# Kernel tuning notes

Hardware: AMD Instinct MI355X
Metric: run time of the kernel (lower is better)

Reference implementation:

```python
import jax, jax.numpy as jnp
import numpy as np

C_S, C_P, FEAT_DIM, NUM_BINS = 256, 128, 64, 22
TOTAL_EDGE_FEATS = FEAT_DIM * 2 + NUM_BINS * 2 + 2  # embed_diffuse_mask=True
LN_EPS = 1e-5


def calc_distogram(pos, min_bin, max_bin, num_bins):
    # pos: [B, N, 3] -> one-hot distance bins [B, N, N, num_bins]
    d = jnp.linalg.norm(pos[:, :, None, :] - pos[:, None, :, :], axis=-1)[..., None]
    lower = jnp.linspace(min_bin, max_bin, num_bins, dtype=pos.dtype)
    upper = jnp.concatenate([lower[1:], jnp.array([1e8], dtype=pos.dtype)])
    return ((d > lower) & (d < upper)).astype(pos.dtype)


def cross_concat(f):
    # f: [B, N, D] -> [B, N, N, 2D]: row-broadcast feats then col-broadcast feats
    B, N, D = f.shape
    fi = jnp.broadcast_to(f[:, :, None, :], (B, N, N, D))
    fj = jnp.broadcast_to(f[:, None, :, :], (B, N, N, D))
    return jnp.concatenate([fi, fj], axis=-1)


def setup_inputs() -> dict:
    key = jax.random.key(0)
    ks = jax.random.split(key, 12)
    B, N = 2, 512
    inp = {
        'init_node_embed': jax.random.normal(ks[0], (B, N, C_S), jnp.float32),
        'trans_t': jax.random.normal(ks[1], (B, N, 3), jnp.float32),
        'trans_sc': jax.random.normal(ks[2], (B, N, 3), jnp.float32),
        'edge_mask': jnp.ones((B, N, N), jnp.float32),
        'diffuse_mask': jnp.ones((B, N), jnp.float32),
        # params (fan-in scaled)
        'Wsp': jax.random.normal(ks[3], (C_S, FEAT_DIM), jnp.float32) / np.sqrt(C_S),
        'bsp': jnp.zeros((FEAT_DIM,), jnp.float32),
        'W1': jax.random.normal(ks[4], (TOTAL_EDGE_FEATS, C_P), jnp.float32) / np.sqrt(TOTAL_EDGE_FEATS),
        'b1': jnp.zeros((C_P,), jnp.float32),
        'W2': jax.random.normal(ks[5], (C_P, C_P), jnp.float32) / np.sqrt(C_P),
        'b2': jnp.zeros((C_P,), jnp.float32),
        'W3': jax.random.normal(ks[6], (C_P, C_P), jnp.float32) / np.sqrt(C_P),
        'b3': jnp.zeros((C_P,), jnp.float32),
        'ln_g': jnp.ones((C_P,), jnp.float32),
        'ln_b': jnp.zeros((C_P,), jnp.float32),
    }
    return inp


def reference(init_node_embed, trans_t, trans_sc, edge_mask, diffuse_mask,
              Wsp, bsp, W1, b1, W2, b2, W3, b3, ln_g, ln_b):
    p_i = init_node_embed @ Wsp + bsp                      # [B,N,feat_dim]
    cross_node = cross_concat(p_i)                          # [B,N,N,2*feat_dim]
    dist_feats = calc_distogram(trans_t, 1e-3, 20.0, NUM_BINS)
    sc_feats = calc_distogram(trans_sc, 1e-3, 20.0, NUM_BINS)
    diff_feat = cross_concat(diffuse_mask[..., None])       # [B,N,N,2]
    feats = jnp.concatenate([cross_node, dist_feats, sc_feats, diff_feat], axis=-1)
    h = jax.nn.relu(feats @ W1 + b1)
    h = jax.nn.relu(h @ W2 + b2)
    h = h @ W3 + b3
    mu = jnp.mean(h, axis=-1, keepdims=True)
    var = jnp.mean(jnp.square(h - mu), axis=-1, keepdims=True)
    h = (h - mu) * jax.lax.rsqrt(var + LN_EPS) * ln_g + ln_b
    return h * edge_mask[..., None]
```

## Files before the change

### kernel.cpp

```cpp
#include <hip/hip_runtime.h>
#include <hip/hip_bf16.h>
#include <math.h>

#define NB 2
#define NN 512
#define CS 256
#define CP 128
#define FD 64
#define NBINS 22
#define EPB 64

typedef __attribute__((ext_vector_type(8))) short bf16x8;
typedef __attribute__((ext_vector_type(4))) short bf16x4;
typedef __attribute__((ext_vector_type(4))) float f32x4;

__device__ __forceinline__ unsigned short f2bf_rne(float x) {
    unsigned int u = __float_as_uint(x);
    unsigned int r = (u + 0x7fffu + ((u >> 16) & 1u)) >> 16;
    return (unsigned short)r;
}
__device__ __forceinline__ float bf2f(unsigned short b) {
    return __uint_as_float(((unsigned int)b) << 16);
}
__device__ __forceinline__ unsigned short f2bf(float x) {
    __hip_bfloat16 h = __float2bfloat16(x);
    unsigned short u;
    __builtin_memcpy(&u, &h, 2);
    return u;
}

__device__ __forceinline__ int bin_of(float d, float step) {
    const float fk = __fdiv_rn(__fsub_rn(d, 0.001f), step);
    int k0 = (int)fk;
    k0 = k0 < 1 ? 1 : (k0 > 20 ? 20 : k0);
    int row = -1;
    #pragma unroll
    for (int dk = -1; dk <= 1; ++dk) {
        const int k = k0 + dk;
        const float lo = __fadd_rn(0.001f, __fmul_rn((float)k, step));
        const float hi = (k == NBINS - 1)
                       ? 1e8f
                       : __fadd_rn(0.001f, __fmul_rn((float)(k + 1), step));
        row = (d > lo && d < hi) ? k : row;
    }
    return row;
}

__global__ __launch_bounds__(256) void ef_prep_kernel(
    const float* __restrict__ x,
    const float* __restrict__ diffuse,
    const float* __restrict__ Wsp,
    const float* __restrict__ bsp,
    const float* __restrict__ W1,
    const float* __restrict__ b1,
    const float* __restrict__ W2,
    const float* __restrict__ W3,
    float* __restrict__ qr,
    unsigned short* __restrict__ Wp)
{
    __shared__ float xs[CS];
    __shared__ float ps[FD];
    const int t = threadIdx.x;
    if (blockIdx.x < 1024) {
        const int n = blockIdx.x;
        xs[t] = x[(size_t)n * CS + t];
        __syncthreads();
        if (t < FD) {
            float acc = bsp[t];
            #pragma unroll 8
            for (int k = 0; k < CS; ++k)
                acc = fmaf(xs[k], Wsp[k * FD + t], acc);
            ps[t] = acc;
        }
        __syncthreads();
        const float dm = diffuse[n];
        const int c = t & (CP - 1);
        if (t < CP) {
            float acc = b1[c] + dm * W1[172 * CP + c];
            #pragma unroll 8
            for (int k = 0; k < FD; ++k)
                acc = fmaf(ps[k], W1[k * CP + c], acc);
            qr[(size_t)n * CP + c] = acc;
        } else {
            float acc = dm * W1[173 * CP + c];
            #pragma unroll 8
            for (int k = 0; k < FD; ++k)
                acc = fmaf(ps[k], W1[(FD + k) * CP + c], acc);
            qr[(size_t)(1024 + n) * CP + c] = acc;
        }
    } else {
        const int s = (blockIdx.x - 1024) * 256 + t;
        const int j    = s & 7;
        const int lane = (s >> 3) & 63;
        const int mt   = (s >> 9) & 7;
        const int ki   = s >> 12;
        const int k = 32 * ki + 8 * (lane >> 4) + j;
        const int n = 16 * mt + (lane & 15);
        const float w2 = W2[k * CP + n];
        const float w3 = W3[k * CP + n];
        const unsigned short h2 = f2bf_rne(w2);
        const unsigned short l2 = f2bf_rne(w2 - bf2f(h2));
        const unsigned short h3 = f2bf_rne(w3);
        const unsigned short l3 = f2bf_rne(w3 - bf2f(h3));
        Wp[s]         = h2;
        Wp[16384 + s] = l2;
        Wp[32768 + s] = h3;
        Wp[49152 + s] = l3;
    }
}

__global__ __launch_bounds__(256, 4) void ef_edge_kernel(
    const float* __restrict__ trans_t,
    const float* __restrict__ trans_sc,
    const float* __restrict__ edge_mask,
    const float* __restrict__ W1,
    const float* __restrict__ b2,
    const float* __restrict__ b3,
    const float* __restrict__ ln_g,
    const float* __restrict__ ln_b,
    const float* __restrict__ qr,
    const unsigned short* __restrict__ Wp,
    float* __restrict__ out)
{
    __shared__ char hb8[32768];
    char* h1buf = hb8;
    char* h2buf = hb8 + 16384;
    float* psum_s  = (float*)hb8;
    float* pqsum_s = (float*)(hb8 + 4352);
    float* mus     = (float*)(hb8 + 8704);
    float* invs    = (float*)(hb8 + 8960);

    const int t   = threadIdx.x;
    const int blk = blockIdx.x;
    const int jt  = blk & 7;
    const int i   = (blk >> 3) & (NN - 1);
    const int b   = blk >> 12;
    const int j0  = jt * EPB;
    const int nodeI  = b * NN + i;
    const int nodeJ0 = b * NN + j0;

    const int w  = t >> 6;
    const int l  = t & 63;
    const int lr = l & 15;
    const int lg = l >> 4;
    const int e1 = t >> 2;
    const int c0 = (t & 3) * 32;
    const int nj = nodeJ0 + e1;

    const float step = __fdiv_rn(__fsub_rn(20.0f, 0.001f), 21.0f);
    float dx = __fsub_rn(trans_t[nodeI * 3 + 0], trans_t[nj * 3 + 0]);
    float dy = __fsub_rn(trans_t[nodeI * 3 + 1], trans_t[nj * 3 + 1]);
    float dz = __fsub_rn(trans_t[nodeI * 3 + 2], trans_t[nj * 3 + 2]);
    const float dT = sqrtf(__fadd_rn(__fadd_rn(__fmul_rn(dx, dx), __fmul_rn(dy, dy)), __fmul_rn(dz, dz)));
    dx = __fsub_rn(trans_sc[nodeI * 3 + 0], trans_sc[nj * 3 + 0]);
    dy = __fsub_rn(trans_sc[nodeI * 3 + 1], trans_sc[nj * 3 + 1]);
    dz = __fsub_rn(trans_sc[nodeI * 3 + 2], trans_sc[nj * 3 + 2]);
    const float dS = sqrtf(__fadd_rn(__fadd_rn(__fmul_rn(dx, dx), __fmul_rn(dy, dy)), __fmul_rn(dz, dz)));
    const int kT = bin_of(dT, step);
    const int kS = bin_of(dS, step);

    {
        const float fT = (kT < 0) ? 0.0f : 1.0f;
        const float fS = (kS < 0) ? 0.0f : 1.0f;
        const float* qrow = qr + (size_t)nodeI * CP + c0;
        const float* rrow = qr + (size_t)(1024 + nj) * CP + c0;
        const float* wTr  = W1 + (size_t)(kT < 0 ? 0 : 128 + kT) * CP + c0;
        const float* wSr  = W1 + (size_t)(kS < 0 ? 0 : 150 + kS) * CP + c0;
        #pragma unroll
        for (int ch = 0; ch < 4; ++ch) {
            const int cc = ch * 8;
            const float4 qa = *(const float4*)(qrow + cc);
            const float4 qb = *(const float4*)(qrow + cc + 4);
            const float4 ra = *(const float4*)(rrow + cc);
            const float4 rb = *(const float4*)(rrow + cc + 4);
            const float4 ta = *(const float4*)(wTr + cc);
            const float4 tb = *(const float4*)(wTr + cc + 4);
            const float4 sa = *(const float4*)(wSr + cc);
            const float4 sb = *(const float4*)(wSr + cc + 4);
            float h[8];
            h[0] = fmaxf(qa.x + ra.x + fT * ta.x + fS * sa.x, 0.0f);
            h[1] = fmaxf(qa.y + ra.y + fT * ta.y + fS * sa.y, 0.0f);
            h[2] = fmaxf(qa.z + ra.z + fT * ta.z + fS * sa.z, 0.0f);
            h[3] = fmaxf(qa.w + ra.w + fT * ta.w + fS * sa.w, 0.0f);
            h[4] = fmaxf(qb.x + rb.x + fT * tb.x + fS * sb.x, 0.0f);
            h[5] = fmaxf(qb.y + rb.y + fT * tb.y + fS * sb.y, 0.0f);
            h[6] = fmaxf(qb.z + rb.z + fT * tb.z + fS * sb.z, 0.0f);
            h[7] = fmaxf(qb.w + rb.w + fT * tb.w + fS * sb.w, 0.0f);
            bf16x8 H;
            #pragma unroll
            for (int u = 0; u < 8; ++u)
                H[u] = (short)f2bf(h[u]);
            const unsigned int ad = (unsigned int)e1 * 256 +
                (((unsigned int)(2 * (c0 + cc))) ^ (((unsigned int)e1 & 7) << 4));
            *(bf16x8*)(h1buf + ad) = H;
        }
    }
    __syncthreads();

    f32x4 acc[2][4];
    #pragma unroll
    for (int mt = 0; mt < 2; ++mt) {
        const float4 bv = *(const float4*)&b2[16 * (2 * w + mt) + 4 * lg];
        #pragma unroll
        for (int nt = 0; nt < 4; ++nt) {
            acc[mt][nt][0] = bv.x; acc[mt][nt][1] = bv.y;
            acc[mt][nt][2] = bv.z; acc[mt][nt][3] = bv.w;
        }
    }
    #pragma unroll
    for (int ki = 0; ki < 4; ++ki) {
        bf16x8 ah[2], al[2];
        #pragma unroll
        for (int mt = 0; mt < 2; ++mt) {
            const size_t off = (((size_t)ki * 8 + (2 * w + mt)) * 64 + l) * 8;
            ah[mt] = *(const bf16x8*)(Wp + off);
            al[mt] = *(const bf16x8*)(Wp + 16384 + off);
        }
        bf16x8 bh[4];
        #pragma unroll
        for (int nt = 0; nt < 4; ++nt) {
            const int e = 16 * nt + lr;
            const unsigned int ad = (unsigned int)e * 256 +
                (((unsigned int)(64 * ki + 16 * lg)) ^ (((unsigned int)e & 7) << 4));
            bh[nt] = *(const bf16x8*)(h1buf + ad);
        }
        __builtin_amdgcn_s_setprio(1);
        #pragma unroll
        for (int mt = 0; mt < 2; ++mt)
            #pragma unroll
            for (int nt = 0; nt < 4; ++nt) {
                acc[mt][nt] = __builtin_amdgcn_mfma_f32_16x16x32_bf16(ah[mt], bh[nt], acc[mt][nt], 0, 0, 0);
                acc[mt][nt] = __builtin_amdgcn_mfma_f32_16x16x32_bf16(al[mt], bh[nt], acc[mt][nt], 0, 0, 0);
            }
        __builtin_amdgcn_s_setprio(0);
    }

    #pragma unroll
    for (int mt = 0; mt < 2; ++mt) {
        const int mtg = 2 * w + mt;
        #pragma unroll
        for (int nt = 0; nt < 4; ++nt) {
            const int e = 16 * nt + lr;
            bf16x4 H;
            H[0] = (short)f2bf(fmaxf(acc[mt][nt][0], 0.0f));
            H[1] = (short)f2bf(fmaxf(acc[mt][nt][1], 0.0f));
            H[2] = (short)f2bf(fmaxf(acc[mt][nt][2], 0.0f));
            H[3] = (short)f2bf(fmaxf(acc[mt][nt][3], 0.0f));
            const unsigned int ad = (unsigned int)e * 256 +
                (((unsigned int)(32 * mtg + 8 * lg)) ^ (((unsigned int)e & 7) << 4));
            *(bf16x4*)(h2buf + ad) = H;
        }
    }
    __syncthreads();

    #pragma unroll
    for (int mt = 0; mt < 2; ++mt) {
        const float4 bv = *(const float4*)&b3[16 * (2 * w + mt) + 4 * lg];
        #pragma unroll
        for (int nt = 0; nt < 4; ++nt) {
            acc[mt][nt][0] = bv.x; acc[mt][nt][1] = bv.y;
            acc[mt][nt][2] = bv.z; acc[mt][nt][3] = bv.w;
        }
    }
    #pragma unroll
    for (int ki = 0; ki < 4; ++ki) {
        bf16x8 ah[2], al[2];
        #pragma unroll
        for (int mt = 0; mt < 2; ++mt) {
            const size_t off = (((size_t)ki * 8 + (2 * w + mt)) * 64 + l) * 8;
            ah[mt] = *(const bf16x8*)(Wp + 32768 + off);
            al[mt] = *(const bf16x8*)(Wp + 49152 + off);
        }
        bf16x8 bh[4];
        #pragma unroll
        for (int nt = 0; nt < 4; ++nt) {
            const int e = 16 * nt + lr;
            const unsigned int ad = (unsigned int)e * 256 +
                (((unsigned int)(64 * ki + 16 * lg)) ^ (((unsigned int)e & 7) << 4));
            bh[nt] = *(const bf16x8*)(h2buf + ad);
        }
        __builtin_amdgcn_s_setprio(1);
        #pragma unroll
        for (int mt = 0; mt < 2; ++mt)
            #pragma unroll
            for (int nt = 0; nt < 4; ++nt) {
                acc[mt][nt] = __builtin_amdgcn_mfma_f32_16x16x32_bf16(ah[mt], bh[nt], acc[mt][nt], 0, 0, 0);
                acc[mt][nt] = __builtin_amdgcn_mfma_f32_16x16x32_bf16(al[mt], bh[nt], acc[mt][nt], 0, 0, 0);
            }
        __builtin_amdgcn_s_setprio(0);
    }

    #pragma unroll
    for (int nt = 0; nt < 4; ++nt) {
        const int e = 16 * nt + lr;
        float s = 0.0f, s2 = 0.0f;
        #pragma unroll
        for (int mt = 0; mt < 2; ++mt)
            #pragma unroll
            for (int r = 0; r < 4; ++r) {
                const float v = acc[mt][nt][r];
                s += v;
                s2 = fmaf(v, v, s2);
            }
        psum_s[e * 17 + 4 * w + lg]  = s;
        pqsum_s[e * 17 + 4 * w + lg] = s2;
    }
    __syncthreads();

    {
        const int e = t & 63;
        float s = 0.0f, s2 = 0.0f;
        #pragma unroll
        for (int k = 0; k < 16; ++k) {
            s  += psum_s[e * 17 + k];
            s2 += pqsum_s[e * 17 + k];
        }
        const float mu  = s * (1.0f / 128.0f);
        const float var = s2 * (1.0f / 128.0f) - mu * mu;
        mus[e]  = mu;
        invs[e] = rsqrtf(var + 1e-5f);
    }
    __syncthreads();

    {
        float4 g4[2], bb4[2];
        #pragma unroll
        for (int mt = 0; mt < 2; ++mt) {
            const int n0 = 16 * (2 * w + mt) + 4 * lg;
            g4[mt]  = *(const float4*)&ln_g[n0];
            bb4[mt] = *(const float4*)&ln_b[n0];
        }
        #pragma unroll
        for (int nt = 0; nt < 4; ++nt) {
            const int e = 16 * nt + lr;
            const size_t erow = ((size_t)(b * NN + i)) * NN + (j0 + e);
            const float em  = edge_mask[erow];
            const float mu  = mus[e];
            const float inv = invs[e];
            float* op = out + erow * CP;
            #pragma unroll
            for (int mt = 0; mt < 2; ++mt) {
                const int n0 = 16 * (2 * w + mt) + 4 * lg;
                float4 o;
                o.x = ((acc[mt][nt][0] - mu) * inv * g4[mt].x + bb4[mt].x) * em;
                o.y = ((acc[mt][nt][1] - mu) * inv * g4[mt].y + bb4[mt].y) * em;
                o.z = ((acc[mt][nt][2] - mu) * inv * g4[mt].z + bb4[mt].z) * em;
                o.w = ((acc[mt][nt][3] - mu) * inv * g4[mt].w + bb4[mt].w) * em;
                *(float4*)(op + n0) = o;
            }
        }
    }
}

extern "C" void kernel_launch(void* const* d_in, const int* in_sizes, int n_in,
                              void* d_out, int out_size, void* d_ws, size_t ws_size,
                              hipStream_t stream) {
    const float* init_node = (const float*)d_in[0];
    const float* trans_t   = (const float*)d_in[1];
    const float* trans_sc  = (const float*)d_in[2];
    const float* edge_mask = (const float*)d_in[3];
    const float* diffuse   = (const float*)d_in[4];
    const float* Wsp       = (const float*)d_in[5];
    const float* bsp       = (const float*)d_in[6];
    const float* W1        = (const float*)d_in[7];
    const float* b1        = (const float*)d_in[8];
    const float* W2        = (const float*)d_in[9];
    const float* b2        = (const float*)d_in[10];
    const float* W3        = (const float*)d_in[11];
    const float* b3        = (const float*)d_in[12];
    const float* ln_g      = (const float*)d_in[13];
    const float* ln_b      = (const float*)d_in[14];
    float* out = (float*)d_out;
    float* qr  = (float*)d_ws;
    unsigned short* Wp = (unsigned short*)((char*)d_ws + (1 << 20));

    ef_prep_kernel<<<1024 + 64, 256, 0, stream>>>(
        init_node, diffuse, Wsp, bsp, W1, b1, W2, W3, qr, Wp);
    ef_edge_kernel<<<NB * NN * (NN / EPB), 256, 0, stream>>>(
        trans_t, trans_sc, edge_mask, W1, b2, b3, ln_g, ln_b, qr, Wp, out);
}
```

Measured before the change: 205.2 us.

## Shrink edge kernel to single-wave blocks of 16 edges each

```diff
diff --git a/kernel.cpp b/kernel.cpp
--- a/kernel.cpp
+++ b/kernel.cpp
@@ -8,7 +8,7 @@
 #define CP 128
 #define FD 64
 #define NBINS 22
-#define EPB 64
+#define EPW 16
 
 typedef __attribute__((ext_vector_type(8))) short bf16x8;
 typedef __attribute__((ext_vector_type(4))) short bf16x4;
@@ -109,7 +109,7 @@
     }
 }
 
-__global__ __launch_bounds__(256, 4) void ef_edge_kernel(
+__global__ __launch_bounds__(64, 4) void ef_edge_kernel(
     const float* __restrict__ trans_t,
     const float* __restrict__ trans_sc,
     const float* __restrict__ edge_mask,
@@ -122,30 +122,25 @@
     const unsigned short* __restrict__ Wp,
     float* __restrict__ out)
 {
-    __shared__ char hb8[32768];
-    char* h1buf = hb8;
-    char* h2buf = hb8 + 16384;
-    float* psum_s  = (float*)hb8;
-    float* pqsum_s = (float*)(hb8 + 4352);
-    float* mus     = (float*)(hb8 + 8704);
-    float* invs    = (float*)(hb8 + 8960);
+    __shared__ char slab[8192];
+    char* h1buf = slab;
+    char* h2buf = slab + 4096;
+    float* psum_s  = (float*)slab;
+    float* pqsum_s = (float*)(slab + 320);
 
     const int t   = threadIdx.x;
     const int blk = blockIdx.x;
-    const int jt  = blk & 7;
-    const int i   = (blk >> 3) & (NN - 1);
-    const int b   = blk >> 12;
-    const int j0  = jt * EPB;
+    const int jt  = blk & 31;
+    const int i   = (blk >> 5) & (NN - 1);
+    const int b   = blk >> 14;
+    const int j0  = jt * EPW;
     const int nodeI  = b * NN + i;
     const int nodeJ0 = b * NN + j0;
 
-    const int w  = t >> 6;
-    const int l  = t & 63;
-    const int lr = l & 15;
-    const int lg = l >> 4;
-    const int e1 = t >> 2;
-    const int c0 = (t & 3) * 32;
-    const int nj = nodeJ0 + e1;
+    const int lr = t & 15;
+    const int lg = t >> 4;
+    const int c0 = lg * 32;
+    const int nj = nodeJ0 + lr;
 
     const float step = __fdiv_rn(__fsub_rn(20.0f, 0.001f), 21.0f);
     float dx = __fsub_rn(trans_t[nodeI * 3 + 0], trans_t[nj * 3 + 0]);
@@ -190,164 +185,127 @@
             #pragma unroll
             for (int u = 0; u < 8; ++u)
                 H[u] = (short)f2bf(h[u]);
-            const unsigned int ad = (unsigned int)e1 * 256 +
-                (((unsigned int)(2 * (c0 + cc))) ^ (((unsigned int)e1 & 7) << 4));
+            const unsigned int ad = (unsigned int)lr * 256 +
+                (((unsigned int)(2 * (c0 + cc))) ^ (((unsigned int)lr & 7) << 4));
             *(bf16x8*)(h1buf + ad) = H;
         }
     }
     __syncthreads();
 
-    f32x4 acc[2][4];
-    #pragma unroll
-    for (int mt = 0; mt < 2; ++mt) {
-        const float4 bv = *(const float4*)&b2[16 * (2 * w + mt) + 4 * lg];
-        #pragma unroll
-        for (int nt = 0; nt < 4; ++nt) {
-            acc[mt][nt][0] = bv.x; acc[mt][nt][1] = bv.y;
-            acc[mt][nt][2] = bv.z; acc[mt][nt][3] = bv.w;
-        }
+    f32x4 acc[8];
+    #pragma unroll
+    for (int mt = 0; mt < 8; ++mt) {
+        const float4 bv = *(const float4*)&b2[16 * mt + 4 * lg];
+        acc[mt][0] = bv.x; acc[mt][1] = bv.y;
+        acc[mt][2] = bv.z; acc[mt][3] = bv.w;
     }
     #pragma unroll
     for (int ki = 0; ki < 4; ++ki) {
-        bf16x8 ah[2], al[2];
-        #pragma unroll
-        for (int mt = 0; mt < 2; ++mt) {
-            const size_t off = (((size_t)ki * 8 + (2 * w + mt)) * 64 + l) * 8;
-            ah[mt] = *(const bf16x8*)(Wp + off);
-            al[mt] = *(const bf16x8*)(Wp + 16384 + off);
-        }
-        bf16x8 bh[4];
-        #pragma unroll
-        for (int nt = 0; nt < 4; ++nt) {
-            const int e = 16 * nt + lr;
-            const unsigned int ad = (unsigned int)e * 256 +
-                (((unsigned int)(64 * ki + 16 * lg)) ^ (((unsigned int)e & 7) << 4));
-            bh[nt] = *(const bf16x8*)(h1buf + ad);
-        }
-        __builtin_amdgcn_s_setprio(1);
-        #pragma unroll
-        for (int mt = 0; mt < 2; ++mt)
-            #pragma unroll
-            for (int nt = 0; nt < 4; ++nt) {
-                acc[mt][nt] = __builtin_amdgcn_mfma_f32_16x16x32_bf16(ah[mt], bh[nt], acc[mt][nt], 0, 0, 0);
-                acc[mt][nt] = __builtin_amdgcn_mfma_f32_16x16x32_bf16(al[mt], bh[nt], acc[mt][nt], 0, 0, 0);
-            }
-        __builtin_amdgcn_s_setprio(0);
-    }
-
-    #pragma unroll
-    for (int mt = 0; mt < 2; ++mt) {
-        const int mtg = 2 * w + mt;
-        #pragma unroll
-        for (int nt = 0; nt < 4; ++nt) {
-            const int e = 16 * nt + lr;
-            bf16x4 H;
-            H[0] = (short)f2bf(fmaxf(acc[mt][nt][0], 0.0f));
-            H[1] = (short)f2bf(fmaxf(acc[mt][nt][1], 0.0f));
-            H[2] = (short)f2bf(fmaxf(acc[mt][nt][2], 0.0f));
-            H[3] = (short)f2bf(fmaxf(acc[mt][nt][3], 0.0f));
-            const unsigned int ad = (unsigned int)e * 256 +
-                (((unsigned int)(32 * mtg + 8 * lg)) ^ (((unsigned int)e & 7) << 4));
-            *(bf16x4*)(h2buf + ad) = H;
-        }
+        const unsigned int ad = (unsigned int)lr * 256 +
+            (((unsigned int)(64 * ki + 16 * lg)) ^ (((unsigned int)lr & 7) << 4));
+        const bf16x8 bh = *(const bf16x8*)(h1buf + ad);
+        #pragma unroll
+        for (int mg = 0; mg < 4; ++mg) {
+            bf16x8 ah[2], al[2];
+            #pragma unroll
+            for (int u = 0; u < 2; ++u) {
+                const size_t off = (((size_t)ki * 8 + (2 * mg + u)) * 64 + t) * 8;
+                ah[u] = *(const bf16x8*)(Wp + off);
+                al[u] = *(const bf16x8*)(Wp + 16384 + off);
+            }
+            __builtin_amdgcn_s_setprio(1);
+            #pragma unroll
+            for (int u = 0; u < 2; ++u) {
+                acc[2 * mg + u] = __builtin_amdgcn_mfma_f32_16x16x32_bf16(ah[u], bh, acc[2 * mg + u], 0, 0, 0);
+                acc[2 * mg + u] = __builtin_amdgcn_mfma_f32_16x16x32_bf16(al[u], bh, acc[2 * mg + u], 0, 0, 0);
+            }
+            __builtin_amdgcn_s_setprio(0);
+        }
+    }
+
+    #pragma unroll
+    for (int mt = 0; mt < 8; ++mt) {
+        bf16x4 H;
+        H[0] = (short)f2bf(fmaxf(acc[mt][0], 0.0f));
+        H[1] = (short)f2bf(fmaxf(acc[mt][1], 0.0f));
+        H[2] = (short)f2bf(fmaxf(acc[mt][2], 0.0f));
+        H[3] = (short)f2bf(fmaxf(acc[mt][3], 0.0f));
+        const unsigned int ad = (unsigned int)lr * 256 +
+            (((unsigned int)(32 * mt + 8 * lg)) ^ (((unsigned int)lr & 7) << 4));
+        *(bf16x4*)(h2buf + ad) = H;
     }
     __syncthreads();
 
     #pragma unroll
-    for (int mt = 0; mt < 2; ++mt) {
-        const float4 bv = *(const float4*)&b3[16 * (2 * w + mt) + 4 * lg];
-        #pragma unroll
-        for (int nt = 0; nt < 4; ++nt) {
-            acc[mt][nt][0] = bv.x; acc[mt][nt][1] = bv.y;
-            acc[mt][nt][2] = bv.z; acc[mt][nt][3] = bv.w;
-        }
+    for (int mt = 0; mt < 8; ++mt) {
+        const float4 bv = *(const float4*)&b3[16 * mt + 4 * lg];
+        acc[mt][0] = bv.x; acc[mt][1] = bv.y;
+        acc[mt][2] = bv.z; acc[mt][3] = bv.w;
     }
     #pragma unroll
     for (int ki = 0; ki < 4; ++ki) {
-        bf16x8 ah[2], al[2];
-        #pragma unroll
-        for (int mt = 0; mt < 2; ++mt) {
-            const size_t off = (((size_t)ki * 8 + (2 * w + mt)) * 64 + l) * 8;
-            ah[mt] = *(const bf16x8*)(Wp + 32768 + off);
-            al[mt] = *(const bf16x8*)(Wp + 49152 + off);
-        }
-        bf16x8 bh[4];
-        #pragma unroll
-        for (int nt = 0; nt < 4; ++nt) {
-            const int e = 16 * nt + lr;
-            const unsigned int ad = (unsigned int)e * 256 +
-                (((unsigned int)(64 * ki + 16 * lg)) ^ (((unsigned int)e & 7) << 4));
-            bh[nt] = *(const bf16x8*)(h2buf + ad);
-        }
-        __builtin_amdgcn_s_setprio(1);
-        #pragma unroll
-        for (int mt = 0; mt < 2; ++mt)
-            #pragma unroll
-            for (int nt = 0; nt < 4; ++nt) {
-                acc[mt][nt] = __builtin_amdgcn_mfma_f32_16x16x32_bf16(ah[mt], bh[nt], acc[mt][nt], 0, 0, 0);
-                acc[mt][nt] = __builtin_amdgcn_mfma_f32_16x16x32_bf16(al[mt], bh[nt], acc[mt][nt], 0, 0, 0);
-            }
-        __builtin_amdgcn_s_setprio(0);
-    }
-
-    #pragma unroll
-    for (int nt = 0; nt < 4; ++nt) {
-        const int e = 16 * nt + lr;
+        const unsigned int ad = (unsigned int)lr * 256 +
+            (((unsigned int)(64 * ki + 16 * lg)) ^ (((unsigned int)lr & 7) << 4));
+        const bf16x8 bh = *(const bf16x8*)(h2buf + ad);
+        #pragma unroll
+        for (int mg = 0; mg < 4; ++mg) {
+            bf16x8 ah[2], al[2];
+            #pragma unroll
+            for (int u = 0; u < 2; ++u) {
+                const size_t off = (((size_t)ki * 8 + (2 * mg + u)) * 64 + t) * 8;
+                ah[u] = *(const bf16x8*)(Wp + 32768 + off);
+                al[u] = *(const bf16x8*)(Wp + 49152 + off);
+            }
+            __builtin_amdgcn_s_setprio(1);
+            #pragma unroll
+            for (int u = 0; u < 2; ++u) {
+                acc[2 * mg + u] = __builtin_amdgcn_mfma_f32_16x16x32_bf16(ah[u], bh, acc[2 * mg + u], 0, 0, 0);
+                acc[2 * mg + u] = __builtin_amdgcn_mfma_f32_16x16x32_bf16(al[u], bh, acc[2 * mg + u], 0, 0, 0);
+            }
+            __builtin_amdgcn_s_setprio(0);
+        }
+    }
+
+    {
         float s = 0.0f, s2 = 0.0f;
         #pragma unroll
-        for (int mt = 0; mt < 2; ++mt)
+        for (int mt = 0; mt < 8; ++mt)
             #pragma unroll
             for (int r = 0; r < 4; ++r) {
-                const float v = acc[mt][nt][r];
+                const float v = acc[mt][r];
                 s += v;
                 s2 = fmaf(v, v, s2);
             }
-        psum_s[e * 17 + 4 * w + lg]  = s;
-        pqsum_s[e * 17 + 4 * w + lg] = s2;
+        psum_s[lr * 5 + lg]  = s;
+        pqsum_s[lr * 5 + lg] = s2;
     }
     __syncthreads();
 
+    float s = 0.0f, s2 = 0.0f;
+    #pragma unroll
+    for (int g = 0; g < 4; ++g) {
+        s  += psum_s[lr * 5 + g];
+        s2 += pqsum_s[lr * 5 + g];
+    }
+    const float mu  = s * (1.0f / 128.0f);
+    const float var = s2 * (1.0f / 128.0f) - mu * mu;
+    const float inv = rsqrtf(var + 1e-5f);
+
     {
-        const int e = t & 63;
-        float s = 0.0f, s2 = 0.0f;
-        #pragma unroll
-        for (int k = 0; k < 16; ++k) {
-            s  += psum_s[e * 17 + k];
-            s2 += pqsum_s[e * 17 + k];
-        }
-        const float mu  = s * (1.0f / 128.0f);
-        const float var = s2 * (1.0f / 128.0f) - mu * mu;
-        mus[e]  = mu;
-        invs[e] = rsqrtf(var + 1e-5f);
-    }
-    __syncthreads();
-
-    {
-        float4 g4[2], bb4[2];
-        #pragma unroll
-        for (int mt = 0; mt < 2; ++mt) {
-            const int n0 = 16 * (2 * w + mt) + 4 * lg;
-            g4[mt]  = *(const float4*)&ln_g[n0];
-            bb4[mt] = *(const float4*)&ln_b[n0];
-        }
-        #pragma unroll
-        for (int nt = 0; nt < 4; ++nt) {
-            const int e = 16 * nt + lr;
-            const size_t erow = ((size_t)(b * NN + i)) * NN + (j0 + e);
-            const float em  = edge_mask[erow];
-            const float mu  = mus[e];
-            const float inv = invs[e];
-            float* op = out + erow * CP;
-            #pragma unroll
-            for (int mt = 0; mt < 2; ++mt) {
-                const int n0 = 16 * (2 * w + mt) + 4 * lg;
-                float4 o;
-                o.x = ((acc[mt][nt][0] - mu) * inv * g4[mt].x + bb4[mt].x) * em;
-                o.y = ((acc[mt][nt][1] - mu) * inv * g4[mt].y + bb4[mt].y) * em;
-                o.z = ((acc[mt][nt][2] - mu) * inv * g4[mt].z + bb4[mt].z) * em;
-                o.w = ((acc[mt][nt][3] - mu) * inv * g4[mt].w + bb4[mt].w) * em;
-                *(float4*)(op + n0) = o;
-            }
+        const size_t erow = ((size_t)(b * NN + i)) * NN + (j0 + lr);
+        const float em = edge_mask[erow];
+        float* op = out + erow * CP;
+        #pragma unroll
+        for (int mt = 0; mt < 8; ++mt) {
+            const int n0 = 16 * mt + 4 * lg;
+            const float4 g4 = *(const float4*)&ln_g[n0];
+            const float4 bb = *(const float4*)&ln_b[n0];
+            float4 o;
+            o.x = ((acc[mt][0] - mu) * inv * g4.x + bb.x) * em;
+            o.y = ((acc[mt][1] - mu) * inv * g4.y + bb.y) * em;
+            o.z = ((acc[mt][2] - mu) * inv * g4.z + bb.z) * em;
+            o.w = ((acc[mt][3] - mu) * inv * g4.w + bb.w) * em;
+            *(float4*)(op + n0) = o;
         }
     }
 }
@@ -376,6 +334,6 @@
 
     ef_prep_kernel<<<1024 + 64, 256, 0, stream>>>(
         init_node, diffuse, Wsp, bsp, W1, b1, W2, W3, qr, Wp);
-    ef_edge_kernel<<<NB * NN * (NN / EPB), 256, 0, stream>>>(
+    ef_edge_kernel<<<NB * NN * (NN / EPW), 64, 0, stream>>>(
         trans_t, trans_sc, edge_mask, W1, b2, b3, ln_g, ln_b, qr, Wp, out);
 }
```

Result: slower. 263.0 us (+28.2%).
